# Kernel optimization log

Measured on AMD Instinct MI355X. Metric: run time of the kernel, lower is better.

Reference implementation:

```python
import jax, jax.numpy as jnp
import numpy as np

ROPE_THETA = 10000.0


def _rotate_half(x):
    # interleaved rotation: out[..., 2i] = -x[..., 2i+1], out[..., 2i+1] = x[..., 2i]
    x_even = x[..., ::2]
    x_odd = x[..., 1::2]
    return jnp.stack([-x_odd, x_even], axis=-1).reshape(x.shape)


def _rope_cos_sin(N, D, dtype):
    inv_freq = 1.0 / (ROPE_THETA ** (jnp.arange(0, D, 2, dtype=jnp.float32) / D))  # [D/2]
    angles = jnp.arange(N, dtype=jnp.float32)[:, None] * inv_freq[None, :]          # [N, D/2]
    angles = jnp.repeat(angles, 2, axis=-1)                                          # [N, D]
    cos = jnp.cos(angles).astype(dtype)[None, :, None, :]  # [1, N, 1, D]
    sin = jnp.sin(angles).astype(dtype)[None, :, None, :]
    return cos, sin


def setup_inputs() -> dict:
    key = jax.random.key(0)
    kq, kk, kv, km = jax.random.split(key, 4)
    B, N, H, D = 16, 1024, 8, 64
    xq = jax.random.normal(kq, (B, N, H, D), dtype=jnp.float32)
    xk = jax.random.normal(kk, (B, N, H, D), dtype=jnp.float32)
    xv = jax.random.normal(kv, (B, N, H, D), dtype=jnp.float32)
    vis_mask = jax.random.bernoulli(km, 0.8, (B, N))  # bool visibility mask per batch
    return {"xq": xq, "xk": xk, "xv": xv, "vis_mask": vis_mask}


def reference(xq, xk, xv, vis_mask):
    B, N, H, D = xq.shape
    sm_scale = 1.0 / np.sqrt(D).astype(np.float32)

    # RoPE (interleaved) on q and k
    cos, sin = _rope_cos_sin(N, D, xq.dtype)
    q = xq * cos + _rotate_half(xq) * sin
    k = xk * cos + _rotate_half(xk) * sin

    # masked full attention: scores [B, H, N, N]
    scores = jnp.einsum("bnhd,bmhd->bhnm", q, k) * sm_scale
    attn_mask = (vis_mask[:, None, :, None] & vis_mask[:, None, None, :])  # [B,1,N,N]
    scores = jnp.where(attn_mask, scores, -jnp.inf)
    p = jax.nn.softmax(scores, axis=-1)
    p = jnp.nan_to_num(p, nan=0.0)  # fully-masked rows -> zeros (matches fallback)
    out = jnp.einsum("bhnm,bmhd->bnhd", p, xv)
    return out
```

## Files before the change

### kernel.cpp

```cpp
#include <hip/hip_runtime.h>
#include <hip/hip_bf16.h>
#include <stdint.h>

#define Bb 16
#define Nn 1024
#define Hh 8
#define Dd 64

typedef unsigned short u16;
typedef float f32x4 __attribute__((ext_vector_type(4)));
typedef short short8 __attribute__((ext_vector_type(8)));

union U4S8 { uint4 u; short8 s; };
union BF2U { __hip_bfloat162 h; uint32_t u; };

__device__ __forceinline__ uint32_t f2bf(float f){
  union{float f;uint32_t i;} v; v.f=f;
  return (v.i + 0x7fffu + ((v.i>>16)&1u))>>16;
}

__device__ __forceinline__ f32x4 mfma16(short8 a, short8 b, f32x4 c){
  return __builtin_amdgcn_mfma_f32_16x16x32_bf16(a,b,c,0,0,0);
}

#define ROPE_K 0.41524101186092030f
#define QS 0.18033688011112042f

__global__ void rope_table_kernel(float2* __restrict__ tab){
  int id = blockIdx.x*256 + threadIdx.x;
  int n = id >> 5, i = id & 31;
  float inv = exp2f(-(float)i * ROPE_K);
  float a = (float)n * inv;
  float s, c; sincosf(a, &s, &c);
  tab[id] = make_float2(c, s);
}

__global__ __launch_bounds__(256) void prepass_kernel(
    const float* __restrict__ xk, const float* __restrict__ xv,
    const float2* __restrict__ tab,
    u16* __restrict__ Kr, u16* __restrict__ Vp)
{
  const int tid = threadIdx.x;
  const int bid = blockIdx.x;
  const int nt = bid & 15, h = (bid>>4)&7, b = bid>>7;
  const size_t bh = (size_t)b*Hh + h;

  {
    int r = tid>>2, c = (tid&3)<<4;
    int n = (nt<<6) + r;
    const float4* g = (const float4*)(xk + ((((size_t)b*Nn + n)*Hh + h)<<6) + c);
    float4 a0=g[0],a1=g[1],a2=g[2],a3=g[3];
    float xx[16] = {a0.x,a0.y,a0.z,a0.w, a1.x,a1.y,a1.z,a1.w,
                    a2.x,a2.y,a2.z,a2.w, a3.x,a3.y,a3.z,a3.w};
    uint32_t w[8];
    #pragma unroll
    for (int j=0;j<8;++j){
      int i = (c>>1)+j;
      float cs, sn;
      if (tab){ float2 t = tab[(n<<5)+i]; cs = t.x; sn = t.y; }
      else { float inv = exp2f(-(float)i * ROPE_K); sincosf((float)n*inv, &sn, &cs); }
      float x0 = xx[2*j], x1 = xx[2*j+1];
      float q0 = x0*cs - x1*sn;
      float q1 = x1*cs + x0*sn;
      w[j] = f2bf(q0) | (f2bf(q1)<<16);
    }
    u16* dst = Kr + (((bh<<10) + (size_t)n)<<6) + c;
    *(uint4*)dst     = make_uint4(w[0],w[1],w[2],w[3]);
    *(uint4*)(dst+8) = make_uint4(w[4],w[5],w[6],w[7]);
  }

  {
    int k = tid&63, ds = (tid>>6)<<4;
    int n = (nt<<6) + k;
    int slot = (k&1) | (((k>>4)&3)<<1) | (((k>>2)&3)<<3) | (((k>>1)&1)<<5);
    const float4* g = (const float4*)(xv + ((((size_t)b*Nn + n)*Hh + h)<<6) + ds);
    float4 a0=g[0],a1=g[1],a2=g[2],a3=g[3];
    float vv[16] = {a0.x,a0.y,a0.z,a0.w, a1.x,a1.y,a1.z,a1.w,
                    a2.x,a2.y,a2.z,a2.w, a3.x,a3.y,a3.z,a3.w};
    #pragma unroll
    for (int j=0;j<16;++j)
      Vp[ (bh<<16) + ((size_t)(ds+j)<<10) + (nt<<6) + slot ] = (u16)f2bf(vv[j]);
  }
}

__global__ __launch_bounds__(256,2) void attn3_kernel(
    const float* __restrict__ xq, const u16* __restrict__ Kr,
    const u16* __restrict__ Vp, const int* __restrict__ vis,
    const float2* __restrict__ tab, float* __restrict__ out)
{
  __shared__ u16 Ks[64][72];
  __shared__ u16 Vs[64][72];

  const int tid  = threadIdx.x;
  const int wave = tid >> 6;
  const int lane = tid & 63;
  const int l15  = lane & 15;
  const int quad = lane >> 4;

  const int bid = blockIdx.x;
  const int qt = bid & 3;
  const int h  = (bid >> 2) & 7;
  const int b  = bid >> 5;
  const size_t bh = (size_t)b*Hh + h;
  const int qbase = qt<<8;

  const int* visb = vis + b*Nn;

  short8 qa[4][2];
  #pragma unroll
  for (int mb=0; mb<4; ++mb){
    int n = qbase + (wave<<6) + (mb<<4) + l15;
    const float* src = xq + ((((size_t)b*Nn + n)*Hh + h)<<6);
    #pragma unroll
    for (int half=0; half<2; ++half){
      int d0 = (half<<5) + (quad<<3);
      const float4* g = (const float4*)(src + d0);
      float4 u0 = g[0], u1 = g[1];
      float xx[8] = {u0.x,u0.y,u0.z,u0.w, u1.x,u1.y,u1.z,u1.w};
      uint32_t w[4];
      #pragma unroll
      for (int j=0;j<4;++j){
        int i = (d0>>1) + j;
        float cs, sn;
        if (tab){ float2 t = tab[(n<<5)+i]; cs = t.x; sn = t.y; }
        else { float inv = exp2f(-(float)i * ROPE_K); sincosf((float)n*inv, &sn, &cs); }
        float x0 = xx[2*j], x1 = xx[2*j+1];
        float q0 = (x0*cs - x1*sn)*QS;
        float q1 = (x1*cs + x0*sn)*QS;
        w[j] = f2bf(q0) | (f2bf(q1)<<16);
      }
      U4S8 t; t.u = make_uint4(w[0],w[1],w[2],w[3]);
      qa[mb][half] = t.s;
    }
  }

  f32x4 acc[4][4];
  float l_r[4];
  #pragma unroll
  for (int mb=0;mb<4;++mb){
    l_r[mb] = 0.f;
    #pragma unroll
    for (int s=0;s<4;++s) acc[mb][s] = (f32x4){0.f,0.f,0.f,0.f};
  }

  const u16* Krb = Kr + (bh<<16);
  const u16* Vpb = Vp + (bh<<16);
  const int r = tid>>2, c16 = (tid&3)<<4;

  for (int kt=0; kt<16; ++kt){
    __syncthreads();
    {
      const u16* ksrc = Krb + ((size_t)((kt<<6)+r)<<6) + c16;
      uint4 k0 = *(const uint4*)ksrc, k1 = *(const uint4*)(ksrc+8);
      const u16* vsrc = Vpb + ((size_t)r<<10) + (kt<<6) + c16;
      uint4 v0 = *(const uint4*)vsrc, v1 = *(const uint4*)(vsrc+8);
      *(uint4*)&Ks[r][c16]   = k0; *(uint4*)&Ks[r][c16+8] = k1;
      *(uint4*)&Vs[r][c16]   = v0; *(uint4*)&Vs[r][c16+8] = v1;
    }
    __syncthreads();

    uint32_t pk[4][2][4];
    #pragma unroll
    for (int kb=0;kb<4;++kb){
      short8 kf0 = *(const short8*)&Ks[(kb<<4)+l15][quad<<3];
      short8 kf1 = *(const short8*)&Ks[(kb<<4)+l15][(quad<<3)+32];
      int4 vi = *(const int4*)&visb[(kt<<6)+(kb<<4)+(quad<<2)];
      float vf0 = vi.x ? 1.f : 0.f;
      float vf1 = vi.y ? 1.f : 0.f;
      float vf2 = vi.z ? 1.f : 0.f;
      float vf3 = vi.w ? 1.f : 0.f;
      #pragma unroll
      for (int mb=0;mb<4;++mb){
        f32x4 t = (f32x4){0.f,0.f,0.f,0.f};
        t = mfma16(kf0, qa[mb][0], t);
        t = mfma16(kf1, qa[mb][1], t);
        float p0 = exp2f(t.x)*vf0;
        float p1 = exp2f(t.y)*vf1;
        float p2 = exp2f(t.z)*vf2;
        float p3 = exp2f(t.w)*vf3;
        l_r[mb] += (p0+p1)+(p2+p3);
        BF2U e0; e0.h = __float22bfloat162_rn(make_float2(p0,p1));
        BF2U e1; e1.h = __float22bfloat162_rn(make_float2(p2,p3));
        pk[kb][0][mb] = e0.u;
        pk[kb][1][mb] = e1.u;
      }
    }

    short8 pa[4][2];
    #pragma unroll
    for (int mb=0;mb<4;++mb){
      U4S8 a0; a0.u = make_uint4(pk[0][0][mb], pk[1][0][mb], pk[2][0][mb], pk[3][0][mb]);
      U4S8 a1; a1.u = make_uint4(pk[0][1][mb], pk[1][1][mb], pk[2][1][mb], pk[3][1][mb]);
      pa[mb][0] = a0.s; pa[mb][1] = a1.s;
    }

    #pragma unroll
    for (int s=0;s<4;++s){
      short8 vb0 = *(const short8*)&Vs[(s<<4)+l15][quad<<3];
      short8 vb1 = *(const short8*)&Vs[(s<<4)+l15][(quad<<3)+32];
      #pragma unroll
      for (int mb=0;mb<4;++mb){
        acc[mb][s] = mfma16(pa[mb][0], vb0, acc[mb][s]);
        acc[mb][s] = mfma16(pa[mb][1], vb1, acc[mb][s]);
      }
    }
  }

  #pragma unroll
  for (int mb=0;mb<4;++mb){
    float lv = l_r[mb];
    lv += __shfl_xor(lv, 16);
    lv += __shfl_xor(lv, 32);
    int4 qvi = *(const int4*)&visb[qbase + (wave<<6) + (mb<<4) + (quad<<2)];
    int qv[4] = {qvi.x, qvi.y, qvi.z, qvi.w};
    #pragma unroll
    for (int rr=0;rr<4;++rr){
      float lq = __shfl(lv, (quad<<2)+rr);
      float invl = (qv[rr] != 0 && lq > 0.f) ? 1.f/lq : 0.f;
      int qrow = qbase + (wave<<6) + (mb<<4) + (quad<<2) + rr;
      float* ob = out + ((((size_t)b*Nn + qrow)*Hh + h)<<6);
      #pragma unroll
      for (int s=0;s<4;++s)
        ob[(s<<4)+l15] = acc[mb][s][rr]*invl;
    }
  }
}

__device__ __forceinline__ void stage_rope_row_fb(const float* __restrict__ src,
                                                  u16 (*dst)[72],
                                                  int n_global, int sr, int d0)
{
  const float4* g = (const float4*)src;
  float4 a0 = g[0], a1 = g[1], a2 = g[2], a3 = g[3];
  float xx[16] = {a0.x,a0.y,a0.z,a0.w, a1.x,a1.y,a1.z,a1.w,
                  a2.x,a2.y,a2.z,a2.w, a3.x,a3.y,a3.z,a3.w};
  uint32_t w[8];
  #pragma unroll
  for (int j=0;j<8;++j){
    int i = (d0>>1)+j;
    float inv = exp2f(-(float)i * ROPE_K);
    float ang = (float)n_global * inv;
    float sn, cs; sincosf(ang, &sn, &cs);
    float x0 = xx[2*j], x1 = xx[2*j+1];
    float q0 = x0*cs - x1*sn;
    float q1 = x1*cs + x0*sn;
    w[j] = f2bf(q0) | (f2bf(q1)<<16);
  }
  *(uint4*)&dst[sr][d0]   = make_uint4(w[0],w[1],w[2],w[3]);
  *(uint4*)&dst[sr][d0+8] = make_uint4(w[4],w[5],w[6],w[7]);
}

__global__ __launch_bounds__(256,2) void attn_fallback(
    const float* __restrict__ xq, const float* __restrict__ xk,
    const float* __restrict__ xv, const int* __restrict__ vis,
    float* __restrict__ out)
{
  __shared__ u16 Qs[64][72];
  __shared__ u16 Ks[64][72];
  __shared__ u16 Vt[64][72];
  __shared__ u16 Ps[4][16][72];
  __shared__ float viss[64];

  const int tid  = threadIdx.x;
  const int wave = tid >> 6;
  const int lane = tid & 63;
  const int l15  = lane & 15;
  const int quad = lane >> 4;

  const int bid = blockIdx.x;
  const int qt = bid & 15;
  const int h  = (bid >> 4) & 7;
  const int b  = bid >> 7;

  const int sr = tid >> 2;
  const int d0 = (tid & 3) << 4;

  {
    int ng = (qt<<6) + sr;
    const float* src = xq + ((((size_t)b*Nn + ng)*Hh + h)<<6) + d0;
    stage_rope_row_fb(src, Qs, ng, sr, d0);
  }
  __syncthreads();

  short8 qa0 = *(const short8*)&Qs[(wave<<4)+l15][quad<<3];
  short8 qa1 = *(const short8*)&Qs[(wave<<4)+l15][(quad<<3)+32];

  f32x4 acc[4];
  #pragma unroll
  for (int s=0;s<4;++s) acc[s] = (f32x4){0.f,0.f,0.f,0.f};
  float m_r[4], l_r[4];
  #pragma unroll
  for (int rr=0;rr<4;++rr){ m_r[rr] = -1e30f; l_r[rr] = 0.f; }

  for (int kt=0; kt<16; ++kt){
    __syncthreads();
    {
      int ng = (kt<<6) + sr;
      const float* src = xk + ((((size_t)b*Nn + ng)*Hh + h)<<6) + d0;
      stage_rope_row_fb(src, Ks, ng, sr, d0);
    }
    {
      int ng = (kt<<6) + sr;
      const float4* g = (const float4*)(xv + ((((size_t)b*Nn + ng)*Hh + h)<<6) + d0);
      float4 a0 = g[0], a1 = g[1], a2 = g[2], a3 = g[3];
      float vv16[16] = {a0.x,a0.y,a0.z,a0.w, a1.x,a1.y,a1.z,a1.w,
                        a2.x,a2.y,a2.z,a2.w, a3.x,a3.y,a3.z,a3.w};
      #pragma unroll
      for (int j=0;j<16;++j) Vt[d0+j][sr] = (u16)f2bf(vv16[j]);
    }
    if (tid < 64) viss[tid] = (vis[b*Nn + (kt<<6) + tid] != 0) ? 1.f : 0.f;
    __syncthreads();

    f32x4 s4[4];
    #pragma unroll
    for (int n=0;n<4;++n){
      short8 kb0 = *(const short8*)&Ks[(n<<4)+l15][quad<<3];
      short8 kb1 = *(const short8*)&Ks[(n<<4)+l15][(quad<<3)+32];
      f32x4 t = (f32x4){0.f,0.f,0.f,0.f};
      t = mfma16(qa0, kb0, t);
      t = mfma16(qa1, kb1, t);
      s4[n] = t;
    }
    float vv[4];
    #pragma unroll
    for (int n=0;n<4;++n) vv[n] = viss[(n<<4)+l15];

    float p[4][4];
    #pragma unroll
    for (int rr=0; rr<4; ++rr){
      float sc[4];
      #pragma unroll
      for (int n=0;n<4;++n) sc[n] = (vv[n] > 0.f) ? s4[n][rr]*0.125f : -1e30f;
      float tm = fmaxf(fmaxf(sc[0],sc[1]), fmaxf(sc[2],sc[3]));
      tm = fmaxf(tm, __shfl_xor(tm,1));
      tm = fmaxf(tm, __shfl_xor(tm,2));
      tm = fmaxf(tm, __shfl_xor(tm,4));
      tm = fmaxf(tm, __shfl_xor(tm,8));
      float mnew  = fmaxf(m_r[rr], tm);
      float alpha = __expf(m_r[rr] - mnew);
      m_r[rr] = mnew;
      float psum = 0.f;
      #pragma unroll
      for (int n=0;n<4;++n){
        float pv = (vv[n] > 0.f) ? __expf(sc[n] - mnew) : 0.f;
        p[n][rr] = pv; psum += pv;
      }
      l_r[rr] = l_r[rr]*alpha + psum;
      #pragma unroll
      for (int s=0;s<4;++s) acc[s][rr] *= alpha;
    }

    #pragma unroll
    for (int n=0;n<4;++n)
      #pragma unroll
      for (int rr=0;rr<4;++rr)
        Ps[wave][(quad<<2)+rr][(n<<4)+l15] = (u16)f2bf(p[n][rr]);
    asm volatile("s_waitcnt lgkmcnt(0)" ::: "memory");
    short8 pa0 = *(const short8*)&Ps[wave][l15][quad<<3];
    short8 pa1 = *(const short8*)&Ps[wave][l15][(quad<<3)+32];

    #pragma unroll
    for (int s=0;s<4;++s){
      short8 vb0 = *(const short8*)&Vt[(s<<4)+l15][quad<<3];
      short8 vb1 = *(const short8*)&Vt[(s<<4)+l15][(quad<<3)+32];
      acc[s] = mfma16(pa0, vb0, acc[s]);
      acc[s] = mfma16(pa1, vb1, acc[s]);
    }
  }

  #pragma unroll
  for (int rr=0;rr<4;++rr){
    float t = l_r[rr];
    t += __shfl_xor(t,1); t += __shfl_xor(t,2);
    t += __shfl_xor(t,4); t += __shfl_xor(t,8);
    int row = (qt<<6) + (wave<<4) + (quad<<2) + rr;
    int qv  = vis[b*Nn + row];
    float invl = (qv != 0 && t > 0.f) ? 1.f/t : 0.f;
    size_t obase = (((size_t)b*Nn + row)*Hh + h) << 6;
    #pragma unroll
    for (int s=0;s<4;++s)
      out[obase + (s<<4) + l15] = acc[s][rr]*invl;
  }
}

extern "C" void kernel_launch(void* const* d_in, const int* in_sizes, int n_in,
                              void* d_out, int out_size, void* d_ws, size_t ws_size,
                              hipStream_t stream)
{
  const float* xq = (const float*)d_in[0];
  const float* xk = (const float*)d_in[1];
  const float* xv = (const float*)d_in[2];
  const int* vis  = (const int*)d_in[3];
  float* out = (float*)d_out;

  const size_t kv_elems = (size_t)Bb*Hh*Nn*Dd;
  const size_t kv_bytes = kv_elems*sizeof(u16);
  const size_t tab_bytes = (size_t)Nn*32*sizeof(float2);
  const size_t need_tab = tab_bytes + 2*kv_bytes;
  const size_t need_kv  = 2*kv_bytes;

  if (d_ws != nullptr && ws_size >= need_tab){
    float2* tab = (float2*)d_ws;
    u16* Kr = (u16*)((char*)d_ws + tab_bytes);
    u16* Vp = Kr + kv_elems;
    rope_table_kernel<<<dim3((Nn*32)/256), dim3(256), 0, stream>>>(tab);
    prepass_kernel<<<dim3(Bb*Hh*(Nn/64)), dim3(256), 0, stream>>>(xk, xv, tab, Kr, Vp);
    attn3_kernel<<<dim3(Bb*Hh*(Nn/256)), dim3(256), 0, stream>>>(xq, Kr, Vp, vis, tab, out);
  } else if (d_ws != nullptr && ws_size >= need_kv){
    u16* Kr = (u16*)d_ws;
    u16* Vp = Kr + kv_elems;
    prepass_kernel<<<dim3(Bb*Hh*(Nn/64)), dim3(256), 0, stream>>>(xk, xv, nullptr, Kr, Vp);
    attn3_kernel<<<dim3(Bb*Hh*(Nn/256)), dim3(256), 0, stream>>>(xq, Kr, Vp, vis, nullptr, out);
  } else {
    attn_fallback<<<dim3(Bb*Hh*(Nn/64)), dim3(256), 0, stream>>>(xq, xk, xv, vis, out);
  }
}
```

Measured before the change: 206.2 us.

## Halve query tile per block, use MFMA for row sums and mask bias

The attention kernel now handles 128 query rows per block instead of 256, doubling the grid and raising launch bounds to 4 blocks per CU to improve occupancy. The visibility mask becomes an additive large-negative bias fed as the MFMA accumulator init, and the fast hardware exp2 replaces the library exp2f. Row sums are computed with an extra MFMA against a ones vector, removing per-element adds and cross-lane shuffles. V is re-laid out tile-contiguously in the prepass so each K/V tile load is a contiguous block. The trade-offs are more blocks re-reading K/V, and a row sum taken from bf16-rounded probabilities.

Measured after the change: 194.2 us. 5.8% less time.

```diff
diff --git a/kernel.cpp b/kernel.cpp
--- a/kernel.cpp
+++ b/kernel.cpp
@@ -25,6 +25,7 @@
 
 #define ROPE_K 0.41524101186092030f
 #define QS 0.18033688011112042f
+#define NEGBIG -1.0e30f
 
 __global__ void rope_table_kernel(float2* __restrict__ tab){
   int id = blockIdx.x*256 + threadIdx.x;
@@ -79,11 +80,11 @@
                     a2.x,a2.y,a2.z,a2.w, a3.x,a3.y,a3.z,a3.w};
     #pragma unroll
     for (int j=0;j<16;++j)
-      Vp[ (bh<<16) + ((size_t)(ds+j)<<10) + (nt<<6) + slot ] = (u16)f2bf(vv[j]);
-  }
-}
-
-__global__ __launch_bounds__(256,2) void attn3_kernel(
+      Vp[ (bh<<16) + (nt<<12) + ((size_t)(ds+j)<<6) + slot ] = (u16)f2bf(vv[j]);
+  }
+}
+
+__global__ __launch_bounds__(256,4) void attn4_kernel(
     const float* __restrict__ xq, const u16* __restrict__ Kr,
     const u16* __restrict__ Vp, const int* __restrict__ vis,
     const float2* __restrict__ tab, float* __restrict__ out)
@@ -98,18 +99,18 @@
   const int quad = lane >> 4;
 
   const int bid = blockIdx.x;
-  const int qt = bid & 3;
-  const int h  = (bid >> 2) & 7;
-  const int b  = bid >> 5;
+  const int qt = bid & 7;
+  const int h  = (bid >> 3) & 7;
+  const int b  = bid >> 6;
   const size_t bh = (size_t)b*Hh + h;
-  const int qbase = qt<<8;
+  const int qbase = qt<<7;
 
   const int* visb = vis + b*Nn;
 
-  short8 qa[4][2];
-  #pragma unroll
-  for (int mb=0; mb<4; ++mb){
-    int n = qbase + (wave<<6) + (mb<<4) + l15;
+  short8 qa[2][2];
+  #pragma unroll
+  for (int mb=0; mb<2; ++mb){
+    int n = qbase + (wave<<5) + (mb<<4) + l15;
     const float* src = xq + ((((size_t)b*Nn + n)*Hh + h)<<6);
     #pragma unroll
     for (int half=0; half<2; ++half){
@@ -134,11 +135,14 @@
     }
   }
 
-  f32x4 acc[4][4];
-  float l_r[4];
-  #pragma unroll
-  for (int mb=0;mb<4;++mb){
-    l_r[mb] = 0.f;
+  U4S8 ones_u; ones_u.u = make_uint4(0x3F803F80u,0x3F803F80u,0x3F803F80u,0x3F803F80u);
+  const short8 ones = ones_u.s;
+
+  f32x4 acc[2][4];
+  f32x4 l_acc[2];
+  #pragma unroll
+  for (int mb=0;mb<2;++mb){
+    l_acc[mb] = (f32x4){0.f,0.f,0.f,0.f};
     #pragma unroll
     for (int s=0;s<4;++s) acc[mb][s] = (f32x4){0.f,0.f,0.f,0.f};
   }
@@ -150,35 +154,34 @@
   for (int kt=0; kt<16; ++kt){
     __syncthreads();
     {
-      const u16* ksrc = Krb + ((size_t)((kt<<6)+r)<<6) + c16;
+      const u16* ksrc = Krb + (kt<<12) + (r<<6) + c16;
       uint4 k0 = *(const uint4*)ksrc, k1 = *(const uint4*)(ksrc+8);
-      const u16* vsrc = Vpb + ((size_t)r<<10) + (kt<<6) + c16;
+      const u16* vsrc = Vpb + (kt<<12) + (r<<6) + c16;
       uint4 v0 = *(const uint4*)vsrc, v1 = *(const uint4*)(vsrc+8);
       *(uint4*)&Ks[r][c16]   = k0; *(uint4*)&Ks[r][c16+8] = k1;
       *(uint4*)&Vs[r][c16]   = v0; *(uint4*)&Vs[r][c16+8] = v1;
     }
     __syncthreads();
 
-    uint32_t pk[4][2][4];
+    uint32_t pk[4][2][2];
     #pragma unroll
     for (int kb=0;kb<4;++kb){
       short8 kf0 = *(const short8*)&Ks[(kb<<4)+l15][quad<<3];
       short8 kf1 = *(const short8*)&Ks[(kb<<4)+l15][(quad<<3)+32];
       int4 vi = *(const int4*)&visb[(kt<<6)+(kb<<4)+(quad<<2)];
-      float vf0 = vi.x ? 1.f : 0.f;
-      float vf1 = vi.y ? 1.f : 0.f;
-      float vf2 = vi.z ? 1.f : 0.f;
-      float vf3 = vi.w ? 1.f : 0.f;
-      #pragma unroll
-      for (int mb=0;mb<4;++mb){
-        f32x4 t = (f32x4){0.f,0.f,0.f,0.f};
-        t = mfma16(kf0, qa[mb][0], t);
+      f32x4 bias;
+      bias.x = vi.x ? 0.f : NEGBIG;
+      bias.y = vi.y ? 0.f : NEGBIG;
+      bias.z = vi.z ? 0.f : NEGBIG;
+      bias.w = vi.w ? 0.f : NEGBIG;
+      #pragma unroll
+      for (int mb=0;mb<2;++mb){
+        f32x4 t = mfma16(kf0, qa[mb][0], bias);
         t = mfma16(kf1, qa[mb][1], t);
-        float p0 = exp2f(t.x)*vf0;
-        float p1 = exp2f(t.y)*vf1;
-        float p2 = exp2f(t.z)*vf2;
-        float p3 = exp2f(t.w)*vf3;
-        l_r[mb] += (p0+p1)+(p2+p3);
+        float p0 = __builtin_amdgcn_exp2f(t.x);
+        float p1 = __builtin_amdgcn_exp2f(t.y);
+        float p2 = __builtin_amdgcn_exp2f(t.z);
+        float p3 = __builtin_amdgcn_exp2f(t.w);
         BF2U e0; e0.h = __float22bfloat162_rn(make_float2(p0,p1));
         BF2U e1; e1.h = __float22bfloat162_rn(make_float2(p2,p3));
         pk[kb][0][mb] = e0.u;
@@ -186,20 +189,25 @@
       }
     }
 
-    short8 pa[4][2];
-    #pragma unroll
-    for (int mb=0;mb<4;++mb){
+    short8 pa[2][2];
+    #pragma unroll
+    for (int mb=0;mb<2;++mb){
       U4S8 a0; a0.u = make_uint4(pk[0][0][mb], pk[1][0][mb], pk[2][0][mb], pk[3][0][mb]);
       U4S8 a1; a1.u = make_uint4(pk[0][1][mb], pk[1][1][mb], pk[2][1][mb], pk[3][1][mb]);
       pa[mb][0] = a0.s; pa[mb][1] = a1.s;
     }
 
     #pragma unroll
+    for (int mb=0;mb<2;++mb){
+      l_acc[mb] = mfma16(pa[mb][0], ones, l_acc[mb]);
+      l_acc[mb] = mfma16(pa[mb][1], ones, l_acc[mb]);
+    }
+    #pragma unroll
     for (int s=0;s<4;++s){
       short8 vb0 = *(const short8*)&Vs[(s<<4)+l15][quad<<3];
       short8 vb1 = *(const short8*)&Vs[(s<<4)+l15][(quad<<3)+32];
       #pragma unroll
-      for (int mb=0;mb<4;++mb){
+      for (int mb=0;mb<2;++mb){
         acc[mb][s] = mfma16(pa[mb][0], vb0, acc[mb][s]);
         acc[mb][s] = mfma16(pa[mb][1], vb1, acc[mb][s]);
       }
@@ -207,17 +215,14 @@
   }
 
   #pragma unroll
-  for (int mb=0;mb<4;++mb){
-    float lv = l_r[mb];
-    lv += __shfl_xor(lv, 16);
-    lv += __shfl_xor(lv, 32);
-    int4 qvi = *(const int4*)&visb[qbase + (wave<<6) + (mb<<4) + (quad<<2)];
+  for (int mb=0;mb<2;++mb){
+    int4 qvi = *(const int4*)&visb[qbase + (wave<<5) + (mb<<4) + (quad<<2)];
     int qv[4] = {qvi.x, qvi.y, qvi.z, qvi.w};
     #pragma unroll
     for (int rr=0;rr<4;++rr){
-      float lq = __shfl(lv, (quad<<2)+rr);
+      float lq = l_acc[mb][rr];
       float invl = (qv[rr] != 0 && lq > 0.f) ? 1.f/lq : 0.f;
-      int qrow = qbase + (wave<<6) + (mb<<4) + (quad<<2) + rr;
+      int qrow = qbase + (wave<<5) + (mb<<4) + (quad<<2) + rr;
       float* ob = out + ((((size_t)b*Nn + qrow)*Hh + h)<<6);
       #pragma unroll
       for (int s=0;s<4;++s)
@@ -405,12 +410,12 @@
     u16* Vp = Kr + kv_elems;
     rope_table_kernel<<<dim3((Nn*32)/256), dim3(256), 0, stream>>>(tab);
     prepass_kernel<<<dim3(Bb*Hh*(Nn/64)), dim3(256), 0, stream>>>(xk, xv, tab, Kr, Vp);
-    attn3_kernel<<<dim3(Bb*Hh*(Nn/256)), dim3(256), 0, stream>>>(xq, Kr, Vp, vis, tab, out);
+    attn4_kernel<<<dim3(Bb*Hh*(Nn/128)), dim3(256), 0, stream>>>(xq, Kr, Vp, vis, tab, out);
   } else if (d_ws != nullptr && ws_size >= need_kv){
     u16* Kr = (u16*)d_ws;
     u16* Vp = Kr + kv_elems;
     prepass_kernel<<<dim3(Bb*Hh*(Nn/64)), dim3(256), 0, stream>>>(xk, xv, nullptr, Kr, Vp);
-    attn3_kernel<<<dim3(Bb*Hh*(Nn/256)), dim3(256), 0, stream>>>(xq, Kr, Vp, vis, nullptr, out);
+    attn4_kernel<<<dim3(Bb*Hh*(Nn/128)), dim3(256), 0, stream>>>(xq, Kr, Vp, vis, nullptr, out);
   } else {
     attn_fallback<<<dim3(Bb*Hh*(Nn/64)), dim3(256), 0, stream>>>(xq, xk, xv, vis, out);
   }
```
